# Optimization experiments

Measured on AMD Instinct MI355X. Metric: run time of the kernel, lower is better.

The kernel has to match this reference:

```python
import jax, jax.numpy as jnp
import numpy as np

N, C, T, V = 128, 256, 48, 25
CR = C // 16
SEG = 3
BN_EPS = 1e-5


def setup_inputs() -> dict:
    key = jax.random.key(0)
    ks = jax.random.split(key, 8)
    s = lambda k, shape: jax.random.normal(k, shape, dtype=jnp.float32) * 0.05
    return {
        "x": jax.random.normal(ks[0], (N, C, T, V), dtype=jnp.float32),
        "w_sq": s(ks[1], (CR, C)),   # me_squeeze 1x1 conv weight [out,in]
        "b_sq": s(ks[2], (CR,)),
        "gamma": jnp.ones((CR,), jnp.float32),   # BN weight
        "beta": jnp.zeros((CR,), jnp.float32),   # BN bias
        "rmean": jnp.zeros((CR,), jnp.float32),  # BN running mean
        "rvar": jnp.ones((CR,), jnp.float32),    # BN running var
        "w_c1": s(ks[3], (CR, CR)),  # me_conv1 1x1 conv weight
        "b_c1": s(ks[4], (CR,)),
        "w_ex": s(ks[5], (C, CR)),   # me_expand 1x1 conv weight
        "b_ex": s(ks[6], (C,)),
    }


def reference(x, w_sq, b_sq, gamma, beta, rmean, rvar, w_c1, b_c1, w_ex, b_ex):
    n, c, t, v = x.shape
    nb = (n * t) // SEG
    cr = w_sq.shape[0]
    # 1x1 squeeze conv + BatchNorm (eval mode, running stats) -> [n, cr, t, v]
    y = jnp.einsum('nctv,rc->nrtv', x, w_sq) + b_sq[None, :, None, None]
    scale = gamma / jnp.sqrt(rvar + BN_EPS)
    y = y * scale[None, :, None, None] + (beta - rmean * scale)[None, :, None, None]
    # 1x1 conv on squeezed features (shifted branch)
    y1 = jnp.einsum('nrtv,sr->nstv', y, w_c1) + b_c1[None, :, None, None]
    # regroup consecutive frames into segments of SEG along time: (n*t) -> (nb, SEG)
    yseg = y.transpose(0, 2, 1, 3).reshape(nb, SEG, cr, v)
    y1seg = y1.transpose(0, 2, 1, 3).reshape(nb, SEG, cr, v)
    # temporal difference: conv(frame k+1) - frame k, zero-pad last frame of each segment
    diff = y1seg[:, 1:] - yseg[:, :SEG - 1]                    # [nb, SEG-1, cr, v]
    diff = jnp.pad(diff, ((0, 0), (0, 1), (0, 0), (0, 0)))     # [nb, SEG, cr, v]
    x_me = diff.reshape(n, t, cr, v).transpose(0, 2, 1, 3)     # [n, cr, t, v]
    # adaptive avg pool over joints (v -> 1), expand conv, sigmoid gate
    m = jnp.mean(x_me, axis=-1, keepdims=True)                 # [n, cr, t, 1]
    gate = jax.nn.sigmoid(jnp.einsum('nrtu,cr->nctu', m, w_ex) + b_ex[None, :, None, None])
    return x * gate
```

## Files before the change

### kernel.cpp

```cpp
#include <hip/hip_runtime.h>

#define N_  128
#define C_  256
#define T_  48
#define V_  25

__global__ __launch_bounds__(512, 4) void k_fused4(
    const float* __restrict__ x,
    const float* __restrict__ wsq, const float* __restrict__ bsq,
    const float* __restrict__ gamma, const float* __restrict__ beta,
    const float* __restrict__ rmean, const float* __restrict__ rvar,
    const float* __restrict__ wc1, const float* __restrict__ bc1,
    const float* __restrict__ wex, const float* __restrict__ bex,
    float* __restrict__ out)
{
    __shared__ float xb[256 * 12];
    __shared__ float part[384];
    __shared__ float ybn[192];
    __shared__ float y1[192];
    __shared__ float mv[192];
    __shared__ float gs[256 * 12];

    const int tid = threadIdx.x;
    const unsigned bid = blockIdx.x;
    const unsigned o   = (bid & 7u) * 64u + (bid >> 3);
    const unsigned n   = o >> 2;
    const unsigned sg  = o & 3u;

    const float* xg = x   + (size_t)n * 307200u + sg * 300u;
    float*       og = out + (size_t)n * 307200u + sg * 300u;

    #pragma unroll
    for (int kk = 0; kk < 3; ++kk) {
        const int fA = (2 * kk) * 512 + tid;
        const int fB = (2 * kk + 1) * 512 + tid;
        const int cA = fA / 12, tA = fA - cA * 12;
        const int cB = fB / 12, tB = fB - cB * 12;
        const int misA = (tA * 25) & 3, misB = (tB * 25) & 3;
        const float4* pA = (const float4*)(xg + (unsigned)(cA * 1200 + tA * 25 - misA));
        const float4* pB = (const float4*)(xg + (unsigned)(cB * 1200 + tB * 25 - misB));
        float4 va[7], vb[7];
        #pragma unroll
        for (int q = 0; q < 7; ++q) va[q] = pA[q];
        #pragma unroll
        for (int q = 0; q < 7; ++q) vb[q] = pB[q];
        float wa[28], wb[28];
        #pragma unroll
        for (int q = 0; q < 7; ++q) {
            wa[4*q] = va[q].x; wa[4*q+1] = va[q].y; wa[4*q+2] = va[q].z; wa[4*q+3] = va[q].w;
            wb[4*q] = vb[q].x; wb[4*q+1] = vb[q].y; wb[4*q+2] = vb[q].z; wb[4*q+3] = vb[q].w;
        }
        float sA = 0.f, sB = 0.f;
        #pragma unroll
        for (int i = 3; i <= 24; ++i) { sA += wa[i]; sB += wb[i]; }
        sA += (misA == 0) ? wa[0] : wa[25];
        sA += (misA <= 1) ? wa[1] : wa[26];
        sA += (misA <= 2) ? wa[2] : wa[27];
        sB += (misB == 0) ? wb[0] : wb[25];
        sB += (misB <= 1) ? wb[1] : wb[26];
        sB += (misB <= 2) ? wb[2] : wb[27];
        xb[fA] = sA * 0.04f;
        xb[fB] = sB * 0.04f;
    }
    __syncthreads();

    if (tid < 384) {
        int t = tid >> 5, rh = tid & 31, r = rh >> 1, h = rh & 1;
        const float* wrow = wsq + r * 256 + h * 128;
        float acc = 0.f;
        #pragma unroll 8
        for (int i = 0; i < 128; ++i) acc += xb[(h * 128 + i) * 12 + t] * wrow[i];
        part[tid] = acc;
    }
    __syncthreads();
    if (tid < 192) {
        int t = tid >> 4, r = tid & 15;
        float acc = part[t * 32 + r * 2] + part[t * 32 + r * 2 + 1];
        float sc = gamma[r] * rsqrtf(rvar[r] + 1e-5f);
        ybn[t * 16 + r] = (acc + bsq[r]) * sc + (beta[r] - rmean[r] * sc);
    }
    __syncthreads();
    if (tid < 192) {
        int t = tid >> 4, s = tid & 15;
        float acc = bc1[s];
        #pragma unroll
        for (int r = 0; r < 16; ++r) acc += ybn[t * 16 + r] * wc1[s * 16 + r];
        y1[t * 16 + s] = acc;
    }
    __syncthreads();
    if (tid < 192) {
        int t = tid >> 4, r = tid & 15;
        mv[tid] = ((t % 3) < 2) ? (y1[(t + 1) * 16 + r] - ybn[t * 16 + r]) : 0.f;
    }
    __syncthreads();
    {
        int c = tid & 255, th = tid >> 8;
        float wexr[16];
        #pragma unroll
        for (int r = 0; r < 16; ++r) wexr[r] = wex[c * 16 + r];
        float be = bex[c];
        #pragma unroll
        for (int t = th * 6; t < th * 6 + 6; ++t) {
            float a = be;
            #pragma unroll
            for (int r = 0; r < 16; ++r) a += mv[t * 16 + r] * wexr[r];
            gs[c * 12 + t] = 1.f / (1.f + expf(-a));
        }
    }
    __syncthreads();

    #pragma unroll 4
    for (int it = 0; it < 38; ++it) {
        int j = it * 512 + tid;
        if (j < 19200) {
            int c = j / 75, pos = j - c * 75;
            const float4 v = *(const float4*)(xg + (unsigned)(c * 1200 + pos * 4));
            int p4  = pos * 4;
            int t0  = (p4 * 41) >> 10;
            int t3  = ((p4 + 3) * 41) >> 10;
            int rem = p4 - t0 * 25;
            float g0 = gs[c * 12 + t0];
            float g3 = gs[c * 12 + t3];
            float4 ov;
            ov.x = v.x * g0;
            ov.y = v.y * ((rem + 1 < 25) ? g0 : g3);
            ov.z = v.z * ((rem + 2 < 25) ? g0 : g3);
            ov.w = v.w * ((rem + 3 < 25) ? g0 : g3);
            *(float4*)(og + (unsigned)(c * 1200 + pos * 4)) = ov;
        }
    }
}

extern "C" void kernel_launch(void* const* d_in, const int* in_sizes, int n_in,
                              void* d_out, int out_size, void* d_ws, size_t ws_size,
                              hipStream_t stream) {
    const float* x     = (const float*)d_in[0];
    const float* wsq   = (const float*)d_in[1];
    const float* bsq   = (const float*)d_in[2];
    const float* gamma = (const float*)d_in[3];
    const float* beta  = (const float*)d_in[4];
    const float* rmean = (const float*)d_in[5];
    const float* rvar  = (const float*)d_in[6];
    const float* wc1   = (const float*)d_in[7];
    const float* bc1   = (const float*)d_in[8];
    const float* wex   = (const float*)d_in[9];
    const float* bex   = (const float*)d_in[10];

    k_fused4<<<512, 512, 0, stream>>>(x, wsq, bsq, gamma, beta,
                                      rmean, rvar, wc1, bc1, wex, bex,
                                      (float*)d_out);
}
```

Baseline: 92.54 us.

## Double-buffer x through LDS with producer warps for the joint-mean reduction

Two producer wavefronts stream the block's x slice into a double-buffered LDS staging area in 16 channel groups, while 192 threads reduce each frame over joints from LDS, replacing the earlier misaligned float4 direct loads. The squeeze matvec is split 8-way with a single-wavefront reduction and folded BN/conv1/diff chain, which cuts barriers. The final gating pass uses a multiply-shift divide and nontemporal stores. Only 128 threads issue loads in the first phase and there are 16 barriers, which may reduce memory-level parallelism. LDS use grows to about 65KB per block, lowering occupancy.

```diff
diff --git a/kernel.cpp b/kernel.cpp
--- a/kernel.cpp
+++ b/kernel.cpp
@@ -5,7 +5,9 @@
 #define T_  48
 #define V_  25
 
-__global__ __launch_bounds__(512, 4) void k_fused4(
+typedef float v4f __attribute__((ext_vector_type(4)));
+
+__global__ __launch_bounds__(512, 4) void k_fused7(
     const float* __restrict__ x,
     const float* __restrict__ wsq, const float* __restrict__ bsq,
     const float* __restrict__ gamma, const float* __restrict__ beta,
@@ -14,93 +16,97 @@
     const float* __restrict__ wex, const float* __restrict__ bex,
     float* __restrict__ out)
 {
-    __shared__ float xb[256 * 12];
-    __shared__ float part[384];
-    __shared__ float ybn[192];
-    __shared__ float y1[192];
-    __shared__ float mv[192];
-    __shared__ float gs[256 * 12];
+    __shared__ v4f   buf[2][1280];
+    __shared__ float xb[3072];
+    __shared__ float gs[3072];
+    __shared__ float ybn[192], y1[192], mv[192];
 
     const int tid = threadIdx.x;
+    const int wv  = tid >> 6;
+    const int ln  = tid & 63;
+
     const unsigned bid = blockIdx.x;
     const unsigned o   = (bid & 7u) * 64u + (bid >> 3);
     const unsigned n   = o >> 2;
-    const unsigned sg  = o & 3u;
+    const unsigned qd  = o & 3u;
 
-    const float* xg = x   + (size_t)n * 307200u + sg * 300u;
-    float*       og = out + (size_t)n * 307200u + sg * 300u;
+    const v4f* x4 = (const v4f*)x + (size_t)n * 76800u + qd * 75u;
+    v4f*       o4 = (v4f*)out     + (size_t)n * 76800u + qd * 75u;
 
-    #pragma unroll
-    for (int kk = 0; kk < 3; ++kk) {
-        const int fA = (2 * kk) * 512 + tid;
-        const int fB = (2 * kk + 1) * 512 + tid;
-        const int cA = fA / 12, tA = fA - cA * 12;
-        const int cB = fB / 12, tB = fB - cB * 12;
-        const int misA = (tA * 25) & 3, misB = (tB * 25) & 3;
-        const float4* pA = (const float4*)(xg + (unsigned)(cA * 1200 + tA * 25 - misA));
-        const float4* pB = (const float4*)(xg + (unsigned)(cB * 1200 + tB * 25 - misB));
-        float4 va[7], vb[7];
+    auto stage = [&](int cg, v4f* dst) {
+        const v4f* xq = x4 + cg * 4800;
+        v4f tmp[10];
         #pragma unroll
-        for (int q = 0; q < 7; ++q) va[q] = pA[q];
+        for (int i = 0; i < 10; ++i) {
+            int s  = i * 128 + (wv - 6) * 64 + ln;
+            int sc = (s < 1200) ? s : 1199;
+            int c  = sc / 75, k = sc - c * 75;
+            tmp[i] = xq[c * 300 + k];
+        }
         #pragma unroll
-        for (int q = 0; q < 7; ++q) vb[q] = pB[q];
-        float wa[28], wb[28];
-        #pragma unroll
-        for (int q = 0; q < 7; ++q) {
-            wa[4*q] = va[q].x; wa[4*q+1] = va[q].y; wa[4*q+2] = va[q].z; wa[4*q+3] = va[q].w;
-            wb[4*q] = vb[q].x; wb[4*q+1] = vb[q].y; wb[4*q+2] = vb[q].z; wb[4*q+3] = vb[q].w;
+        for (int i = 0; i < 10; ++i)
+            dst[i * 128 + (wv - 6) * 64 + ln] = tmp[i];
+    };
+
+    if (wv >= 6) stage(0, buf[0]);
+    __syncthreads();
+    for (int cg = 0; cg < 16; ++cg) {
+        if (wv >= 6 && cg < 15) stage(cg + 1, buf[(cg + 1) & 1]);
+        if (tid < 192) {
+            int cl = tid / 12, t = tid - cl * 12;
+            const float* bp = (const float*)&buf[cg & 1][cl * 75] + t * 25;
+            float s = 0.f;
+            #pragma unroll
+            for (int v = 0; v < 25; ++v) s += bp[v];
+            xb[(cg * 16 + cl) * 12 + t] = s;
         }
-        float sA = 0.f, sB = 0.f;
-        #pragma unroll
-        for (int i = 3; i <= 24; ++i) { sA += wa[i]; sB += wb[i]; }
-        sA += (misA == 0) ? wa[0] : wa[25];
-        sA += (misA <= 1) ? wa[1] : wa[26];
-        sA += (misA <= 2) ? wa[2] : wa[27];
-        sB += (misB == 0) ? wb[0] : wb[25];
-        sB += (misB <= 1) ? wb[1] : wb[26];
-        sB += (misB <= 2) ? wb[2] : wb[27];
-        xb[fA] = sA * 0.04f;
-        xb[fB] = sB * 0.04f;
+        __syncthreads();
+    }
+
+    for (int e = tid; e < 1536; e += 512) {
+        int g = e & 7, q = e >> 3, t = q >> 4, r = q & 15;
+        const float* wrow = wsq + r * 256 + g * 32;
+        float acc = 0.f;
+        #pragma unroll 8
+        for (int i = 0; i < 32; ++i) acc += xb[(g * 32 + i) * 12 + t] * wrow[i];
+        gs[e] = acc;
     }
     __syncthreads();
 
-    if (tid < 384) {
-        int t = tid >> 5, rh = tid & 31, r = rh >> 1, h = rh & 1;
-        const float* wrow = wsq + r * 256 + h * 128;
-        float acc = 0.f;
-        #pragma unroll 8
-        for (int i = 0; i < 128; ++i) acc += xb[(h * 128 + i) * 12 + t] * wrow[i];
-        part[tid] = acc;
+    if (wv == 0) {
+        #pragma unroll
+        for (int j = 0; j < 3; ++j) {
+            int q = ln + j * 64, r = q & 15;
+            float acc = 0.f;
+            #pragma unroll
+            for (int g = 0; g < 8; ++g) acc += gs[q * 8 + g];
+            float sc = gamma[r] * rsqrtf(rvar[r] + 1e-5f);
+            ybn[q] = acc * (0.04f * sc) + (bsq[r] * sc + beta[r] - rmean[r] * sc);
+        }
+        #pragma unroll
+        for (int j = 0; j < 3; ++j) {
+            int q = ln + j * 64, t = q >> 4, s = q & 15;
+            float acc = bc1[s];
+            #pragma unroll
+            for (int r = 0; r < 16; ++r) acc += ybn[t * 16 + r] * wc1[s * 16 + r];
+            y1[q] = acc;
+        }
+        #pragma unroll
+        for (int j = 0; j < 3; ++j) {
+            int q = ln + j * 64, t = q >> 4;
+            mv[q] = ((t % 3) < 2) ? (y1[q + 16] - ybn[q]) : 0.f;
+        }
     }
     __syncthreads();
-    if (tid < 192) {
-        int t = tid >> 4, r = tid & 15;
-        float acc = part[t * 32 + r * 2] + part[t * 32 + r * 2 + 1];
-        float sc = gamma[r] * rsqrtf(rvar[r] + 1e-5f);
-        ybn[t * 16 + r] = (acc + bsq[r]) * sc + (beta[r] - rmean[r] * sc);
-    }
-    __syncthreads();
-    if (tid < 192) {
-        int t = tid >> 4, s = tid & 15;
-        float acc = bc1[s];
-        #pragma unroll
-        for (int r = 0; r < 16; ++r) acc += ybn[t * 16 + r] * wc1[s * 16 + r];
-        y1[t * 16 + s] = acc;
-    }
-    __syncthreads();
-    if (tid < 192) {
-        int t = tid >> 4, r = tid & 15;
-        mv[tid] = ((t % 3) < 2) ? (y1[(t + 1) * 16 + r] - ybn[t * 16 + r]) : 0.f;
-    }
-    __syncthreads();
+
     {
-        int c = tid & 255, th = tid >> 8;
+        int c = tid & 255, half = tid >> 8;
         float wexr[16];
         #pragma unroll
         for (int r = 0; r < 16; ++r) wexr[r] = wex[c * 16 + r];
         float be = bex[c];
         #pragma unroll
-        for (int t = th * 6; t < th * 6 + 6; ++t) {
+        for (int t = half * 6; t < half * 6 + 6; ++t) {
             float a = be;
             #pragma unroll
             for (int r = 0; r < 16; ++r) a += mv[t * 16 + r] * wexr[r];
@@ -113,20 +119,21 @@
     for (int it = 0; it < 38; ++it) {
         int j = it * 512 + tid;
         if (j < 19200) {
-            int c = j / 75, pos = j - c * 75;
-            const float4 v = *(const float4*)(xg + (unsigned)(c * 1200 + pos * 4));
-            int p4  = pos * 4;
-            int t0  = (p4 * 41) >> 10;
-            int t3  = ((p4 + 3) * 41) >> 10;
-            int rem = p4 - t0 * 25;
+            unsigned c = ((unsigned)j * 55926u) >> 22;
+            int k = j - (int)c * 75;
+            v4f v = x4[c * 300 + k];
+            int m0  = k * 4;
+            int t0  = (m0 * 41) >> 10;
+            int t3  = ((m0 + 3) * 41) >> 10;
+            int rem = m0 - t0 * 25;
             float g0 = gs[c * 12 + t0];
             float g3 = gs[c * 12 + t3];
-            float4 ov;
+            v4f ov;
             ov.x = v.x * g0;
             ov.y = v.y * ((rem + 1 < 25) ? g0 : g3);
             ov.z = v.z * ((rem + 2 < 25) ? g0 : g3);
             ov.w = v.w * ((rem + 3 < 25) ? g0 : g3);
-            *(float4*)(og + (unsigned)(c * 1200 + pos * 4)) = ov;
+            __builtin_nontemporal_store(ov, &o4[c * 300 + k]);
         }
     }
 }
@@ -146,7 +153,7 @@
     const float* wex   = (const float*)d_in[9];
     const float* bex   = (const float*)d_in[10];
 
-    k_fused4<<<512, 512, 0, stream>>>(x, wsq, bsq, gamma, beta,
+    k_fused7<<<512, 512, 0, stream>>>(x, wsq, bsq, gamma, beta,
                                       rmean, rvar, wc1, bc1, wex, bex,
                                       (float*)d_out);
 }
```

Result: faster. 85.59 us (-7.5%).
